# Kernel optimization log

Measured on AMD Instinct MI355X. Metric: run time of the kernel, lower is better.

## Reference

```python
import jax, jax.numpy as jnp
import numpy as np
import math

D, H, NQP, NKP = 512, 8, 4, 4
DH = D // H
OUT_DIM = D + H * NKP * 3  # 608


def setup_inputs() -> dict:
    key = jax.random.key(0)
    ks = jax.random.split(key, 12)
    B, L = 2, 1024
    s = jax.random.normal(ks[0], (B, L, D), dtype=jnp.float32)
    R = jax.random.normal(ks[1], (B, L, 3, 3), dtype=jnp.float32)
    tr = jax.random.normal(ks[2], (B, L, 3), dtype=jnp.float32)
    sc = 0.02
    Wq = jax.random.normal(ks[3], (D, D), dtype=jnp.float32) * sc
    Wk = jax.random.normal(ks[4], (D, D), dtype=jnp.float32) * sc
    Wv = jax.random.normal(ks[5], (D, D), dtype=jnp.float32) * sc
    Wqp = jax.random.normal(ks[6], (D, H * NQP * 3), dtype=jnp.float32) * sc
    Wkp = jax.random.normal(ks[7], (D, H * NKP * 3), dtype=jnp.float32) * sc
    Wvp = jax.random.normal(ks[8], (D, H * NKP * 3), dtype=jnp.float32) * sc
    Wo = jax.random.normal(ks[9], (OUT_DIM, D), dtype=jnp.float32) * sc
    bo = jnp.zeros((D,), dtype=jnp.float32)
    gamma = jnp.ones((D,), dtype=jnp.float32)
    beta = jnp.zeros((D,), dtype=jnp.float32)
    w_C = jnp.full((H,), math.log(20.0), dtype=jnp.float32)
    return dict(s=s, R=R, tr=tr, Wq=Wq, Wk=Wk, Wv=Wv, Wqp=Wqp, Wkp=Wkp,
                Wvp=Wvp, Wo=Wo, bo=bo, gamma=gamma, beta=beta, w_C=w_C)


def _layernorm(x, gamma, beta, eps=1e-5):
    mu = jnp.mean(x, axis=-1, keepdims=True)
    var = jnp.var(x, axis=-1, keepdims=True)
    return (x - mu) * jax.lax.rsqrt(var + eps) * gamma + beta


def reference(s, R, tr, Wq, Wk, Wv, Wqp, Wkp, Wvp, Wo, bo, gamma, beta, w_C):
    B, L, _ = s.shape
    # scalar q/k/v: (B, L, H, dh)
    Q = (s @ Wq).reshape(B, L, H, DH)
    K = (s @ Wk).reshape(B, L, H, DH)
    V = (s @ Wv).reshape(B, L, H, DH)
    a_s = jnp.einsum('bihd,bjhd->bhij', Q, K) / math.sqrt(DH)
    # local points: (B, L, H, P, 3)
    Qp = (s @ Wqp).reshape(B, L, H, NQP, 3)
    Kp = (s @ Wkp).reshape(B, L, H, NKP, 3)
    Vp = (s @ Wvp).reshape(B, L, H, NKP, 3)
    tr_e = tr[:, :, None, None, :]
    to_global = lambda p: jnp.einsum('blxy,blhpy->blhpx', R, p) + tr_e
    Qp_g, Kp_g, Vp_g = to_global(Qp), to_global(Kp), to_global(Vp)
    # (B, H, L, P, 3)
    qh = jnp.transpose(Qp_g, (0, 2, 1, 3, 4))
    kh = jnp.transpose(Kp_g, (0, 2, 1, 3, 4))
    diff = qh[:, :, :, None] - kh[:, :, None]          # (B,H,L,L,P,3)
    sq_dist = jnp.sum(diff * diff, axis=(-2, -1))      # (B,H,L,L)
    wc = jax.nn.softplus(w_C)[None, :, None, None]
    attn = jax.nn.softmax(a_s - 0.5 * wc * sq_dist, axis=-1)
    out_s = jnp.einsum('bhij,bjhd->bihd', attn, V).reshape(B, L, D)
    Vp_agg = jnp.einsum('bhij,bjhpc->bihpc', attn, Vp_g)  # (B,L,H,P,3)
    # global -> local: R^T (p - tr)
    Vp_local = jnp.einsum('blyx,blhpy->blhpx', R, Vp_agg - tr_e)
    out_p = Vp_local.reshape(B, L, H * NKP * 3)
    out = jnp.concatenate([out_s, out_p], axis=-1) @ Wo + bo
    return _layernorm(s + out, gamma, beta)
```

## Files before the change

### kernel.cpp

```cpp
#include <hip/hip_runtime.h>
#include <hip/hip_fp16.h>
#include <math.h>

typedef _Float16 f16;
typedef _Float16 f16x8 __attribute__((ext_vector_type(8)));
typedef _Float16 f16x4v __attribute__((ext_vector_type(4)));
typedef float f32x4 __attribute__((ext_vector_type(4)));

#define BATCH   2
#define LSEQ    1024
#define BLTOT   2048
#define DMODEL  512
#define NHEAD   8
#define PDIM    1824
#define AW      96
#define VW      80
#define ODIM    608
#define NSPLIT  2
#define OCPSTR  1310720

__global__ __launch_bounds__(256)
void prep_kernel(const float* __restrict__ s,
                 const float* __restrict__ Wq, const float* __restrict__ Wk,
                 const float* __restrict__ Wv, const float* __restrict__ Wqp,
                 const float* __restrict__ Wkp, const float* __restrict__ Wvp,
                 const float* __restrict__ Wo,
                 f16* __restrict__ sH, f16* __restrict__ WallT, f16* __restrict__ WoT)
{
    const int blk = blockIdx.x;
    const int t = threadIdx.x;
    __shared__ float tile[32][33];

    if (blk < 1024) {
        const int i = blk * 256 + t;
        float4 v = ((const float4*)s)[i];
        f16x4v o = { (f16)v.x, (f16)v.y, (f16)v.z, (f16)v.w };
        ((f16x4v*)sH)[i] = o;
        return;
    }
    if (blk < 1936) {
        const int idx = blk - 1024;
        const int n0 = (idx % 57) * 32, k0 = (idx / 57) * 32;
        const float* src; int ld, nc0;
        if      (n0 < 512)  { src = Wq;  ld = 512; nc0 = n0; }
        else if (n0 < 1024) { src = Wk;  ld = 512; nc0 = n0 - 512; }
        else if (n0 < 1536) { src = Wv;  ld = 512; nc0 = n0 - 1024; }
        else if (n0 < 1632) { src = Wqp; ld = 96;  nc0 = n0 - 1536; }
        else if (n0 < 1728) { src = Wkp; ld = 96;  nc0 = n0 - 1632; }
        else                { src = Wvp; ld = 96;  nc0 = n0 - 1728; }
#pragma unroll
        for (int i = 0; i < 4; ++i) {
            const int idx2 = t + i * 256;
            const int kl = idx2 >> 5, nl = idx2 & 31;
            tile[kl][nl] = src[(long long)(k0 + kl) * ld + nc0 + nl];
        }
        __syncthreads();
#pragma unroll
        for (int i = 0; i < 4; ++i) {
            const int idx2 = t + i * 256;
            const int nl = idx2 >> 5, kl = idx2 & 31;
            WallT[(long long)(n0 + nl) * 512 + k0 + kl] = (f16)tile[kl][nl];
        }
        return;
    }
    {
        const int idx = blk - 1936;
        const int n0 = (idx % 16) * 32, k0 = (idx / 16) * 32;
#pragma unroll
        for (int i = 0; i < 4; ++i) {
            const int idx2 = t + i * 256;
            const int kl = idx2 >> 5, nl = idx2 & 31;
            tile[kl][nl] = Wo[(long long)(k0 + kl) * 512 + n0 + nl];
        }
        __syncthreads();
#pragma unroll
        for (int i = 0; i < 4; ++i) {
            const int idx2 = t + i * 256;
            const int nl = idx2 >> 5, kl = idx2 & 31;
            WoT[(long long)(n0 + nl) * 608 + k0 + kl] = (f16)tile[kl][nl];
        }
    }
}

template<int BN, bool OUT16>
__global__ __launch_bounds__(256)
void gemm2_kernel(const f16* __restrict__ A, const f16* __restrict__ Bt,
                  void* __restrict__ Cout, int K, int ldc)
{
    constexpr int BCH = (BN * 4 + 255) / 256;
    __shared__ f16 As[2][64][40];
    __shared__ f16 Bs[2][BN][40];
    const int t = threadIdx.x;
    const int w = t >> 6, lane = t & 63, l15 = lane & 15, lhi = lane >> 4;
    const int row0 = blockIdx.y * 64, col0 = blockIdx.x * BN;
    const int ar = t >> 2, ac = t & 3;

    f32x4 acc[BN / 16];
#pragma unroll
    for (int n = 0; n < BN / 16; ++n) acc[n] = (f32x4){0.f, 0.f, 0.f, 0.f};

    const int nsteps = K >> 5;

    f16x8 aR;
    f16x8 bR[BCH];
    aR = *(const f16x8*)&A[(long long)(row0 + ar) * K + ac * 8];
#pragma unroll
    for (int i = 0; i < BCH; ++i) {
        const int cid = t + i * 256;
        if (cid < BN * 4) {
            const int br = cid >> 2, bc = cid & 3;
            bR[i] = *(const f16x8*)&Bt[(long long)(col0 + br) * K + bc * 8];
        }
    }
    *(f16x8*)&As[0][ar][ac * 8] = aR;
#pragma unroll
    for (int i = 0; i < BCH; ++i) {
        const int cid = t + i * 256;
        if (cid < BN * 4) *(f16x8*)&Bs[0][cid >> 2][(cid & 3) * 8] = bR[i];
    }
    __syncthreads();

    for (int st = 0; st < nsteps; ++st) {
        const int cur = st & 1;
        if (st + 1 < nsteps) {
            const int k0 = (st + 1) << 5;
            aR = *(const f16x8*)&A[(long long)(row0 + ar) * K + k0 + ac * 8];
#pragma unroll
            for (int i = 0; i < BCH; ++i) {
                const int cid = t + i * 256;
                if (cid < BN * 4) {
                    const int br = cid >> 2, bc = cid & 3;
                    bR[i] = *(const f16x8*)&Bt[(long long)(col0 + br) * K + k0 + bc * 8];
                }
            }
        }
        f16x8 af = *(const f16x8*)&As[cur][w * 16 + l15][lhi * 8];
        f16x8 bf[BN / 16];
#pragma unroll
        for (int n = 0; n < BN / 16; ++n)
            bf[n] = *(const f16x8*)&Bs[cur][n * 16 + l15][lhi * 8];
#pragma unroll
        for (int n = 0; n < BN / 16; ++n)
            acc[n] = __builtin_amdgcn_mfma_f32_16x16x32_f16(af, bf[n], acc[n], 0, 0, 0);
        if (st + 1 < nsteps) {
            *(f16x8*)&As[cur ^ 1][ar][ac * 8] = aR;
#pragma unroll
            for (int i = 0; i < BCH; ++i) {
                const int cid = t + i * 256;
                if (cid < BN * 4) *(f16x8*)&Bs[cur ^ 1][cid >> 2][(cid & 3) * 8] = bR[i];
            }
        }
        __syncthreads();
    }

    const int row = row0 + w * 16 + lhi * 4;
#pragma unroll
    for (int n = 0; n < BN / 16; ++n) {
        const int col = col0 + n * 16 + l15;
#pragma unroll
        for (int r = 0; r < 4; ++r) {
            if (OUT16) ((f16*)Cout)[(long long)(row + r) * ldc + col] = (f16)acc[n][r];
            else       ((float*)Cout)[(long long)(row + r) * ldc + col] = acc[n][r];
        }
    }
}

__global__ __launch_bounds__(256)
void build_aug2_kernel(const f16* __restrict__ P, const float* __restrict__ Rm,
                       const float* __restrict__ tr, const float* __restrict__ wC,
                       f16* __restrict__ QA, f16* __restrict__ KA,
                       f16* __restrict__ VCT, float* __restrict__ KOFF)
{
    const int l0 = blockIdx.x * 64;
    const int bh = blockIdx.y;
    const int b = bh >> 3, h = bh & 7;
    const int t = threadIdx.x;

    __shared__ float Rl[64][9];
    __shared__ float trl[64][3];
    __shared__ f16 gq[64][12];
    __shared__ f16 gk[64][12];
    __shared__ float k2[64][4];
    __shared__ f16 Vt[VW][72];
    __shared__ float wcs;

    const long long blbase = (long long)b * LSEQ + l0;

    for (int i = t; i < 64 * 9; i += 256) Rl[i / 9][i % 9] = Rm[blbase * 9 + i];
    for (int i = t; i < 64 * 3; i += 256) trl[i / 3][i % 3] = tr[blbase * 3 + i];
    if (t == 0) { float x = wC[h]; wcs = log1pf(expf(x)); }
    __syncthreads();
    const float wc = wcs;

    for (int i = t; i < 768; i += 256) {
        const int l = i / 12, pp = i - l * 12;
        const int proj = pp >> 2, p = pp & 3;
        const f16* src = P + (blbase + l) * PDIM + 1536 + proj * 96 + h * 12 + p * 3;
        const float x = (float)src[0], y = (float)src[1], z = (float)src[2];
        const float gx = Rl[l][0]*x + Rl[l][1]*y + Rl[l][2]*z + trl[l][0];
        const float gy = Rl[l][3]*x + Rl[l][4]*y + Rl[l][5]*z + trl[l][1];
        const float gz = Rl[l][6]*x + Rl[l][7]*y + Rl[l][8]*z + trl[l][2];
        if (proj == 0) {
            gq[l][p * 3 + 0] = (f16)(wc * gx);
            gq[l][p * 3 + 1] = (f16)(wc * gy);
            gq[l][p * 3 + 2] = (f16)(wc * gz);
        } else if (proj == 1) {
            gk[l][p * 3 + 0] = (f16)gx;
            gk[l][p * 3 + 1] = (f16)gy;
            gk[l][p * 3 + 2] = (f16)gz;
            k2[l][p] = gx * gx + gy * gy + gz * gz;
        } else {
            Vt[64 + p * 3 + 0][l] = (f16)gx;
            Vt[64 + p * 3 + 1][l] = (f16)gy;
            Vt[64 + p * 3 + 2][l] = (f16)gz;
        }
    }
    for (int i = t; i < 512; i += 256) {
        const int l = i >> 3, ch = i & 7;
        f16x8 v = *(const f16x8*)&P[(blbase + l) * PDIM + 1024 + h * 64 + ch * 8];
#pragma unroll
        for (int j = 0; j < 8; ++j) Vt[ch * 8 + j][l] = v[j];
    }
    for (int i = t; i < 36; i += 256) {
        const int r = 76 + i / 9, ch = i % 9;
        *(f16x8*)&Vt[r][ch * 8] = (f16x8){0,0,0,0,0,0,0,0};
    }
    __syncthreads();

    if (t < 64)
        KOFF[(long long)bh * LSEQ + l0 + t] =
            0.5f * wc * (k2[t][0] + k2[t][1] + k2[t][2] + k2[t][3]);

    for (int i = t; i < 768; i += 256) {
        const int l = i / 12, ch = i - l * 12;
        const long long prow = (blbase + l) * PDIM;
        const long long orow = ((long long)bh * LSEQ + l0 + l) * AW;
        f16x8 q, k;
        if (ch < 8) {
            f16x8 qv = *(const f16x8*)&P[prow + h * 64 + ch * 8];
            f16x8 kv = *(const f16x8*)&P[prow + 512 + h * 64 + ch * 8];
            q = qv * (f16)0.125f;
            k = kv;
        } else if (ch == 8) {
#pragma unroll
            for (int j = 0; j < 8; ++j) { q[j] = gq[l][j]; k[j] = gk[l][j]; }
        } else if (ch == 9) {
#pragma unroll
            for (int j = 0; j < 8; ++j) {
                q[j] = (j < 4) ? gq[l][8 + j] : (f16)0.f;
                k[j] = (j < 4) ? gk[l][8 + j] : (f16)0.f;
            }
        } else {
            q = (f16x8){0,0,0,0,0,0,0,0};
            k = (f16x8){0,0,0,0,0,0,0,0};
        }
        *(f16x8*)&QA[orow + ch * 8] = q;
        *(f16x8*)&KA[orow + ch * 8] = k;
    }
    for (int i = t; i < 640; i += 256) {
        const int c = i >> 3, lg = i & 7;
        *(f16x8*)&VCT[((long long)bh * VW + c) * LSEQ + l0 + lg * 8] =
            *(const f16x8*)&Vt[c][lg * 8];
    }
}

__global__ __launch_bounds__(256, 2)
void attn_kernel(const f16* __restrict__ QA, const f16* __restrict__ KA,
                 const f16* __restrict__ VCT, const float* __restrict__ KOFF,
                 f16* __restrict__ OCp, float2* __restrict__ ML)
{
    const int bh = blockIdx.y;
    const int q0 = blockIdx.x * 64;
    const int z  = blockIdx.z;
    const int t = threadIdx.x;
    const int w = t >> 6, lane = t & 63, l15 = lane & 15, lhi = lane >> 4;

    __shared__ f16 Ks[128][104];
    __shared__ f16 Vs[VW][136];
    __shared__ f16 Ps[64][136];

    const f16* qbase = QA + ((long long)bh * LSEQ + q0 + w * 16 + l15) * AW;
    f16x8 qf[3];
#pragma unroll
    for (int ks = 0; ks < 3; ++ks)
        qf[ks] = *(const f16x8*)(qbase + ks * 32 + lhi * 8);

    f32x4 Oacc[5];
#pragma unroll
    for (int nv = 0; nv < 5; ++nv) Oacc[nv] = (f32x4){0.f, 0.f, 0.f, 0.f};
    float M[4], L[4];
#pragma unroll
    for (int r = 0; r < 4; ++r) { M[r] = -1e30f; L[r] = 0.f; }

    const f16* kgbase = KA + (long long)bh * LSEQ * AW;
    const f16* vgbase = VCT + (long long)bh * VW * LSEQ;
    const float* koffb = KOFF + (long long)bh * LSEQ;

    const int kvbeg = z * (LSEQ / NSPLIT);
    const int kvend = kvbeg + LSEQ / NSPLIT;

#pragma unroll
    for (int i = 0; i < 6; ++i) {
        const int cid = t + i * 256;
        const int r = cid / 12, c = cid - r * 12;
        *(f16x8*)&Ks[r][c * 8] = *(const f16x8*)(kgbase + (long long)(kvbeg + r) * AW + c * 8);
    }
#pragma unroll
    for (int i = 0; i < 5; ++i) {
        const int cid = t + i * 256;
        const int r = cid >> 4, c = cid & 15;
        *(f16x8*)&Vs[r][c * 8] = *(const f16x8*)(vgbase + (long long)r * LSEQ + kvbeg + c * 8);
    }
    __syncthreads();

    for (int kv0 = kvbeg; kv0 < kvend; kv0 += 128) {
        const bool more = (kv0 + 128 < kvend);
        f16x8 kpre[6], vpre[5];
        if (more) {
#pragma unroll
            for (int i = 0; i < 6; ++i) {
                const int cid = t + i * 256;
                const int r = cid / 12, c = cid - r * 12;
                kpre[i] = *(const f16x8*)(kgbase + (long long)(kv0 + 128 + r) * AW + c * 8);
            }
#pragma unroll
            for (int i = 0; i < 5; ++i) {
                const int cid = t + i * 256;
                const int r = cid >> 4, c = cid & 15;
                vpre[i] = *(const f16x8*)(vgbase + (long long)r * LSEQ + kv0 + 128 + c * 8);
            }
        }

        f32x4 sc[8];
#pragma unroll
        for (int n = 0; n < 8; ++n) sc[n] = (f32x4){0.f, 0.f, 0.f, 0.f};
        __builtin_amdgcn_s_setprio(1);
#pragma unroll
        for (int n = 0; n < 8; ++n)
#pragma unroll
            for (int ks = 0; ks < 3; ++ks) {
                f16x8 kb = *(const f16x8*)&Ks[n * 16 + l15][ks * 32 + lhi * 8];
                sc[n] = __builtin_amdgcn_mfma_f32_16x16x32_f16(qf[ks], kb, sc[n], 0, 0, 0);
            }
        __builtin_amdgcn_s_setprio(0);
#pragma unroll
        for (int n = 0; n < 8; ++n) {
            const float ko = koffb[kv0 + n * 16 + l15];
#pragma unroll
            for (int r = 0; r < 4; ++r) sc[n][r] -= ko;
        }
        float sscale[4];
#pragma unroll
        for (int r = 0; r < 4; ++r) {
            float mr = sc[0][r];
#pragma unroll
            for (int n = 1; n < 8; ++n) mr = fmaxf(mr, sc[n][r]);
#pragma unroll
            for (int off = 1; off < 16; off <<= 1) mr = fmaxf(mr, __shfl_xor(mr, off));
            const float nm = fmaxf(M[r], mr);
            sscale[r] = __expf(M[r] - nm);
            M[r] = nm;
        }
        float rsum[4] = {0.f, 0.f, 0.f, 0.f};
#pragma unroll
        for (int n = 0; n < 8; ++n)
#pragma unroll
            for (int r = 0; r < 4; ++r) {
                const float p = __expf(sc[n][r] - M[r]);
                sc[n][r] = p;
                rsum[r] += p;
            }
#pragma unroll
        for (int r = 0; r < 4; ++r) {
            float s = rsum[r];
#pragma unroll
            for (int off = 1; off < 16; off <<= 1) s += __shfl_xor(s, off);
            L[r] = L[r] * sscale[r] + s;
        }
#pragma unroll
        for (int nv = 0; nv < 5; ++nv)
#pragma unroll
            for (int r = 0; r < 4; ++r) Oacc[nv][r] *= sscale[r];

#pragma unroll
        for (int n = 0; n < 8; ++n)
#pragma unroll
            for (int r = 0; r < 4; ++r)
                Ps[w * 16 + lhi * 4 + r][n * 16 + l15] = (f16)sc[n][r];

        f16x8 pa[4];
#pragma unroll
        for (int ks = 0; ks < 4; ++ks)
            pa[ks] = *(const f16x8*)&Ps[w * 16 + l15][ks * 32 + lhi * 8];
        __builtin_amdgcn_s_setprio(1);
#pragma unroll
        for (int nv = 0; nv < 5; ++nv)
#pragma unroll
            for (int ks = 0; ks < 4; ++ks) {
                f16x8 vb = *(const f16x8*)&Vs[nv * 16 + l15][ks * 32 + lhi * 8];
                Oacc[nv] = __builtin_amdgcn_mfma_f32_16x16x32_f16(pa[ks], vb, Oacc[nv], 0, 0, 0);
            }
        __builtin_amdgcn_s_setprio(0);
        __syncthreads();

        if (more) {
#pragma unroll
            for (int i = 0; i < 6; ++i) {
                const int cid = t + i * 256;
                const int r = cid / 12, c = cid - r * 12;
                *(f16x8*)&Ks[r][c * 8] = kpre[i];
            }
#pragma unroll
            for (int i = 0; i < 5; ++i) {
                const int cid = t + i * 256;
                const int r = cid >> 4, c = cid & 15;
                *(f16x8*)&Vs[r][c * 8] = vpre[i];
            }
        }
        __syncthreads();
    }

    f16* obase = OCp + (((long long)(z * 16 + bh) * LSEQ) + q0 + w * 16 + lhi * 4) * VW;
#pragma unroll
    for (int nv = 0; nv < 5; ++nv)
#pragma unroll
        for (int r = 0; r < 4; ++r)
            obase[r * VW + nv * 16 + l15] = (f16)Oacc[nv][r];
    if (l15 == 0) {
#pragma unroll
        for (int r = 0; r < 4; ++r)
            ML[(long long)(z * 16 + bh) * LSEQ + q0 + w * 16 + lhi * 4 + r] =
                make_float2(M[r], L[r]);
    }
}

__global__ __launch_bounds__(256)
void combine_concat_kernel(const f16* __restrict__ OCp, const float2* __restrict__ ML,
                           const float* __restrict__ Rm, const float* __restrict__ tr,
                           f16* __restrict__ CC)
{
    const int bl0 = blockIdx.x * 4;
    const int b = bl0 >> 10;
    const int t = threadIdx.x;

    __shared__ float w1s[4][8], w2s[4][8];
    if (t < 32) {
        const int row = t >> 3, h = t & 7;
        const int l = (bl0 + row) & 1023;
        const int bh = b * 8 + h;
        const float2 m1 = ML[(long long)bh * LSEQ + l];
        const float2 m2 = ML[(long long)(16 + bh) * LSEQ + l];
        const float mm = fmaxf(m1.x, m2.x);
        const float e1 = __expf(m1.x - mm), e2 = __expf(m2.x - mm);
        const float inv = 1.0f / (m1.y * e1 + m2.y * e2);
        w1s[row][h] = e1 * inv; w2s[row][h] = e2 * inv;
    }
    __syncthreads();

    for (int idx = t; idx < 2048; idx += 256) {
        const int row = idx >> 9, c = idx & 511;
        const int h = c >> 6, ch = c & 63;
        const int l = (bl0 + row) & 1023;
        const long long base = ((long long)(b * 8 + h) * LSEQ + l) * VW + ch;
        const float v = w1s[row][h] * (float)OCp[base] + w2s[row][h] * (float)OCp[OCPSTR + base];
        CC[(long long)(bl0 + row) * ODIM + c] = (f16)v;
    }
    if (t < 128) {
        const int row = t >> 5, h = (t >> 2) & 7, p = t & 3;
        const int bl = bl0 + row, l = bl & 1023;
        const long long base = ((long long)(b * 8 + h) * LSEQ + l) * VW + 64 + p * 3;
        const float w1 = w1s[row][h], w2 = w2s[row][h];
        float o[3];
#pragma unroll
        for (int c = 0; c < 3; ++c)
            o[c] = w1 * (float)OCp[base + c] + w2 * (float)OCp[OCPSTR + base + c]
                 - tr[(long long)bl * 3 + c];
        const float* Rr = Rm + (long long)bl * 9;
        f16* crow = CC + (long long)bl * ODIM + 512 + h * 12 + p * 3;
        crow[0] = (f16)(Rr[0]*o[0] + Rr[3]*o[1] + Rr[6]*o[2]);
        crow[1] = (f16)(Rr[1]*o[0] + Rr[4]*o[1] + Rr[7]*o[2]);
        crow[2] = (f16)(Rr[2]*o[0] + Rr[5]*o[1] + Rr[8]*o[2]);
    }
}

__global__ __launch_bounds__(256)
void residual_ln_kernel(const float* __restrict__ s, const float* __restrict__ Y,
                        const float* __restrict__ bo, const float* __restrict__ gamma,
                        const float* __restrict__ beta, float* __restrict__ out)
{
    const int bl = blockIdx.x;
    const int t = threadIdx.x;
    const float* srow = s + (long long)bl * DMODEL;
    const float* yrow = Y + (long long)bl * DMODEL;

    const float v0 = srow[t]       + yrow[t]       + bo[t];
    const float v1 = srow[t + 256] + yrow[t + 256] + bo[t + 256];

    float sum = v0 + v1, sq = v0 * v0 + v1 * v1;
#pragma unroll
    for (int o = 32; o > 0; o >>= 1) {
        sum += __shfl_xor(sum, o);
        sq  += __shfl_xor(sq,  o);
    }
    __shared__ float rs[4], rq[4];
    const int wid = t >> 6, lane = t & 63;
    if (lane == 0) { rs[wid] = sum; rq[wid] = sq; }
    __syncthreads();
    sum = rs[0] + rs[1] + rs[2] + rs[3];
    sq  = rq[0] + rq[1] + rq[2] + rq[3];

    const float mu  = sum * (1.0f / DMODEL);
    const float var = sq * (1.0f / DMODEL) - mu * mu;
    const float inv = rsqrtf(var + 1e-5f);

    out[(long long)bl * DMODEL + t]       = (v0 - mu) * inv * gamma[t]       + beta[t];
    out[(long long)bl * DMODEL + t + 256] = (v1 - mu) * inv * gamma[t + 256] + beta[t + 256];
}

extern "C" void kernel_launch(void* const* d_in, const int* in_sizes, int n_in,
                              void* d_out, int out_size, void* d_ws, size_t ws_size,
                              hipStream_t stream)
{
    const float* s    = (const float*)d_in[0];
    const float* R    = (const float*)d_in[1];
    const float* tr   = (const float*)d_in[2];
    const float* Wq   = (const float*)d_in[3];
    const float* Wk   = (const float*)d_in[4];
    const float* Wv   = (const float*)d_in[5];
    const float* Wqp  = (const float*)d_in[6];
    const float* Wkp  = (const float*)d_in[7];
    const float* Wvp  = (const float*)d_in[8];
    const float* Wo   = (const float*)d_in[9];
    const float* bo   = (const float*)d_in[10];
    const float* gam  = (const float*)d_in[11];
    const float* bet  = (const float*)d_in[12];
    const float* wC   = (const float*)d_in[13];
    float* out = (float*)d_out;

    f16* sH    = (f16*)d_ws;
    f16* WallT = sH + 1048576;
    f16* WoT   = WallT + 933888;
    f16* P     = WoT + 311296;
    f16* QA    = P + 3735552;
    f16* KA    = QA + 1572864;
    f16* VCT   = KA + 1572864;
    float* KOFF = (float*)(VCT + 1310720);
    f16* OCp    = (f16*)(KOFF + 16384);
    float2* ML  = (float2*)(OCp + 2621440);
    f16* CC     = (f16*)(ML + 32768);
    float* Y    = (float*)(CC + 1245184);

    const dim3 blk(256);

    prep_kernel<<<dim3(2240), blk, 0, stream>>>(s, Wq, Wk, Wv, Wqp, Wkp, Wvp, Wo,
                                                sH, WallT, WoT);

    gemm2_kernel<96, true><<<dim3(19, 32), blk, 0, stream>>>(sH, WallT, P, 512, 1824);

    build_aug2_kernel<<<dim3(16, 16), blk, 0, stream>>>(P, R, tr, wC, QA, KA, VCT, KOFF);

    attn_kernel<<<dim3(16, 16, NSPLIT), blk, 0, stream>>>(QA, KA, VCT, KOFF, OCp, ML);

    combine_concat_kernel<<<dim3(512), blk, 0, stream>>>(OCp, ML, R, tr, CC);

    gemm2_kernel<64, false><<<dim3(8, 32), blk, 0, stream>>>(CC, WoT, Y, 608, 512);

    residual_ln_kernel<<<dim3(BLTOT), blk, 0, stream>>>(s, Y, bo, gam, bet, out);
}
```

Baseline: 72.69 us.

## Fuse fp32-to-fp16 conversion into projection GEMM, add lazy softmax rescale, LSE combine

Removes the separate s-to-fp16 pass by loading fp32 s directly inside a new 128x96-tile projection GEMM. The attention kernel skips the running-max rescale when the new block max stays within 8 of the current max, normalizes its output in-kernel and writes log-sum-exp instead of (max, sum) pairs, which simplifies the split combine. The output GEMM is replaced with a 2x2-warp-tiled kernel. These changes cut kernel work and memory traffic, at the cost of more registers in the projection GEMM and a warp-divergent branch in the softmax loop.

```diff
diff --git a/kernel.cpp b/kernel.cpp
--- a/kernel.cpp
+++ b/kernel.cpp
@@ -20,27 +20,18 @@
 #define OCPSTR  1310720
 
 __global__ __launch_bounds__(256)
-void prep_kernel(const float* __restrict__ s,
-                 const float* __restrict__ Wq, const float* __restrict__ Wk,
+void prep_kernel(const float* __restrict__ Wq, const float* __restrict__ Wk,
                  const float* __restrict__ Wv, const float* __restrict__ Wqp,
                  const float* __restrict__ Wkp, const float* __restrict__ Wvp,
                  const float* __restrict__ Wo,
-                 f16* __restrict__ sH, f16* __restrict__ WallT, f16* __restrict__ WoT)
+                 f16* __restrict__ WallT, f16* __restrict__ WoT)
 {
     const int blk = blockIdx.x;
     const int t = threadIdx.x;
     __shared__ float tile[32][33];
 
-    if (blk < 1024) {
-        const int i = blk * 256 + t;
-        float4 v = ((const float4*)s)[i];
-        f16x4v o = { (f16)v.x, (f16)v.y, (f16)v.z, (f16)v.w };
-        ((f16x4v*)sH)[i] = o;
-        return;
-    }
-    if (blk < 1936) {
-        const int idx = blk - 1024;
-        const int n0 = (idx % 57) * 32, k0 = (idx / 57) * 32;
+    if (blk < 912) {
+        const int n0 = (blk % 57) * 32, k0 = (blk / 57) * 32;
         const float* src; int ld, nc0;
         if      (n0 < 512)  { src = Wq;  ld = 512; nc0 = n0; }
         else if (n0 < 1024) { src = Wk;  ld = 512; nc0 = n0 - 512; }
@@ -64,7 +55,7 @@
         return;
     }
     {
-        const int idx = blk - 1936;
+        const int idx = blk - 912;
         const int n0 = (idx % 16) * 32, k0 = (idx / 16) * 32;
 #pragma unroll
         for (int i = 0; i < 4; ++i) {
@@ -82,85 +73,114 @@
     }
 }
 
-template<int BN, bool OUT16>
 __global__ __launch_bounds__(256)
-void gemm2_kernel(const f16* __restrict__ A, const f16* __restrict__ Bt,
-                  void* __restrict__ Cout, int K, int ldc)
-{
-    constexpr int BCH = (BN * 4 + 255) / 256;
-    __shared__ f16 As[2][64][40];
-    __shared__ f16 Bs[2][BN][40];
+void proj_kernel(const float* __restrict__ s, const f16* __restrict__ WallT,
+                 f16* __restrict__ P)
+{
+    __shared__ f16 As[2][128][40];
+    __shared__ f16 Bs[2][96][40];
     const int t = threadIdx.x;
     const int w = t >> 6, lane = t & 63, l15 = lane & 15, lhi = lane >> 4;
-    const int row0 = blockIdx.y * 64, col0 = blockIdx.x * BN;
-    const int ar = t >> 2, ac = t & 3;
-
-    f32x4 acc[BN / 16];
-#pragma unroll
-    for (int n = 0; n < BN / 16; ++n) acc[n] = (f32x4){0.f, 0.f, 0.f, 0.f};
-
-    const int nsteps = K >> 5;
-
-    f16x8 aR;
-    f16x8 bR[BCH];
-    aR = *(const f16x8*)&A[(long long)(row0 + ar) * K + ac * 8];
-#pragma unroll
-    for (int i = 0; i < BCH; ++i) {
+    const int row0 = blockIdx.y * 128, col0 = blockIdx.x * 96;
+
+    f32x4 acc[2][6];
+#pragma unroll
+    for (int m = 0; m < 2; ++m)
+#pragma unroll
+        for (int n = 0; n < 6; ++n) acc[m][n] = (f32x4){0.f, 0.f, 0.f, 0.f};
+
+    float4 aR[2][2];
+    f16x8 bR[2];
+
+#pragma unroll
+    for (int i = 0; i < 2; ++i) {
         const int cid = t + i * 256;
-        if (cid < BN * 4) {
+        const int r = cid >> 2, c = cid & 3;
+        aR[i][0] = *(const float4*)&s[(long long)(row0 + r) * 512 + c * 8];
+        aR[i][1] = *(const float4*)&s[(long long)(row0 + r) * 512 + c * 8 + 4];
+    }
+#pragma unroll
+    for (int i = 0; i < 2; ++i) {
+        const int cid = t + i * 256;
+        if (cid < 384) {
             const int br = cid >> 2, bc = cid & 3;
-            bR[i] = *(const f16x8*)&Bt[(long long)(col0 + br) * K + bc * 8];
-        }
-    }
-    *(f16x8*)&As[0][ar][ac * 8] = aR;
-#pragma unroll
-    for (int i = 0; i < BCH; ++i) {
+            bR[i] = *(const f16x8*)&WallT[(long long)(col0 + br) * 512 + bc * 8];
+        }
+    }
+#pragma unroll
+    for (int i = 0; i < 2; ++i) {
         const int cid = t + i * 256;
-        if (cid < BN * 4) *(f16x8*)&Bs[0][cid >> 2][(cid & 3) * 8] = bR[i];
+        const int r = cid >> 2, c = cid & 3;
+        f16x8 v = { (f16)aR[i][0].x, (f16)aR[i][0].y, (f16)aR[i][0].z, (f16)aR[i][0].w,
+                    (f16)aR[i][1].x, (f16)aR[i][1].y, (f16)aR[i][1].z, (f16)aR[i][1].w };
+        *(f16x8*)&As[0][r][c * 8] = v;
+    }
+#pragma unroll
+    for (int i = 0; i < 2; ++i) {
+        const int cid = t + i * 256;
+        if (cid < 384) *(f16x8*)&Bs[0][cid >> 2][(cid & 3) * 8] = bR[i];
     }
     __syncthreads();
 
-    for (int st = 0; st < nsteps; ++st) {
+    for (int st = 0; st < 16; ++st) {
         const int cur = st & 1;
-        if (st + 1 < nsteps) {
+        if (st + 1 < 16) {
             const int k0 = (st + 1) << 5;
-            aR = *(const f16x8*)&A[(long long)(row0 + ar) * K + k0 + ac * 8];
-#pragma unroll
-            for (int i = 0; i < BCH; ++i) {
-                const int cid = t + i * 256;
-                if (cid < BN * 4) {
+#pragma unroll
+            for (int i = 0; i < 2; ++i) {
+                const int cid = t + i * 256;
+                const int r = cid >> 2, c = cid & 3;
+                aR[i][0] = *(const float4*)&s[(long long)(row0 + r) * 512 + k0 + c * 8];
+                aR[i][1] = *(const float4*)&s[(long long)(row0 + r) * 512 + k0 + c * 8 + 4];
+            }
+#pragma unroll
+            for (int i = 0; i < 2; ++i) {
+                const int cid = t + i * 256;
+                if (cid < 384) {
                     const int br = cid >> 2, bc = cid & 3;
-                    bR[i] = *(const f16x8*)&Bt[(long long)(col0 + br) * K + k0 + bc * 8];
+                    bR[i] = *(const f16x8*)&WallT[(long long)(col0 + br) * 512 + k0 + bc * 8];
                 }
             }
         }
-        f16x8 af = *(const f16x8*)&As[cur][w * 16 + l15][lhi * 8];
-        f16x8 bf[BN / 16];
-#pragma unroll
-        for (int n = 0; n < BN / 16; ++n)
+        f16x8 af[2], bf[6];
+#pragma unroll
+        for (int m = 0; m < 2; ++m)
+            af[m] = *(const f16x8*)&As[cur][w * 32 + m * 16 + l15][lhi * 8];
+#pragma unroll
+        for (int n = 0; n < 6; ++n)
             bf[n] = *(const f16x8*)&Bs[cur][n * 16 + l15][lhi * 8];
 #pragma unroll
-        for (int n = 0; n < BN / 16; ++n)
-            acc[n] = __builtin_amdgcn_mfma_f32_16x16x32_f16(af, bf[n], acc[n], 0, 0, 0);
-        if (st + 1 < nsteps) {
-            *(f16x8*)&As[cur ^ 1][ar][ac * 8] = aR;
-#pragma unroll
-            for (int i = 0; i < BCH; ++i) {
-                const int cid = t + i * 256;
-                if (cid < BN * 4) *(f16x8*)&Bs[cur ^ 1][cid >> 2][(cid & 3) * 8] = bR[i];
+        for (int m = 0; m < 2; ++m)
+#pragma unroll
+            for (int n = 0; n < 6; ++n)
+                acc[m][n] = __builtin_amdgcn_mfma_f32_16x16x32_f16(af[m], bf[n], acc[m][n], 0, 0, 0);
+        if (st + 1 < 16) {
+#pragma unroll
+            for (int i = 0; i < 2; ++i) {
+                const int cid = t + i * 256;
+                const int r = cid >> 2, c = cid & 3;
+                f16x8 v = { (f16)aR[i][0].x, (f16)aR[i][0].y, (f16)aR[i][0].z, (f16)aR[i][0].w,
+                            (f16)aR[i][1].x, (f16)aR[i][1].y, (f16)aR[i][1].z, (f16)aR[i][1].w };
+                *(f16x8*)&As[cur ^ 1][r][c * 8] = v;
+            }
+#pragma unroll
+            for (int i = 0; i < 2; ++i) {
+                const int cid = t + i * 256;
+                if (cid < 384) *(f16x8*)&Bs[cur ^ 1][cid >> 2][(cid & 3) * 8] = bR[i];
             }
         }
         __syncthreads();
     }
 
-    const int row = row0 + w * 16 + lhi * 4;
-#pragma unroll
-    for (int n = 0; n < BN / 16; ++n) {
-        const int col = col0 + n * 16 + l15;
-#pragma unroll
-        for (int r = 0; r < 4; ++r) {
-            if (OUT16) ((f16*)Cout)[(long long)(row + r) * ldc + col] = (f16)acc[n][r];
-            else       ((float*)Cout)[(long long)(row + r) * ldc + col] = acc[n][r];
+#pragma unroll
+    for (int m = 0; m < 2; ++m) {
+        const int row = row0 + w * 32 + m * 16 + lhi * 4;
+#pragma unroll
+        for (int n = 0; n < 6; ++n) {
+            const int col = col0 + n * 16 + l15;
+#pragma unroll
+            for (int r = 0; r < 4; ++r)
+                P[(long long)(row + r) * PDIM + col] = (f16)acc[m][n][r];
         }
     }
 }
@@ -267,7 +287,7 @@
 __global__ __launch_bounds__(256, 2)
 void attn_kernel(const f16* __restrict__ QA, const f16* __restrict__ KA,
                  const f16* __restrict__ VCT, const float* __restrict__ KOFF,
-                 f16* __restrict__ OCp, float2* __restrict__ ML)
+                 f16* __restrict__ OCp, float* __restrict__ LSE)
 {
     const int bh = blockIdx.y;
     const int q0 = blockIdx.x * 64;
@@ -349,38 +369,63 @@
 #pragma unroll
             for (int r = 0; r < 4; ++r) sc[n][r] -= ko;
         }
-        float sscale[4];
+        float mr[4];
 #pragma unroll
         for (int r = 0; r < 4; ++r) {
-            float mr = sc[0][r];
-#pragma unroll
-            for (int n = 1; n < 8; ++n) mr = fmaxf(mr, sc[n][r]);
-#pragma unroll
-            for (int off = 1; off < 16; off <<= 1) mr = fmaxf(mr, __shfl_xor(mr, off));
-            const float nm = fmaxf(M[r], mr);
-            sscale[r] = __expf(M[r] - nm);
-            M[r] = nm;
-        }
+            float m = sc[0][r];
+#pragma unroll
+            for (int n = 1; n < 8; ++n) m = fmaxf(m, sc[n][r]);
+#pragma unroll
+            for (int off = 1; off < 16; off <<= 1) m = fmaxf(m, __shfl_xor(m, off));
+            mr[r] = m;
+        }
+        const bool nog = (mr[0] <= M[0] + 8.f) && (mr[1] <= M[1] + 8.f) &&
+                         (mr[2] <= M[2] + 8.f) && (mr[3] <= M[3] + 8.f);
         float rsum[4] = {0.f, 0.f, 0.f, 0.f};
-#pragma unroll
-        for (int n = 0; n < 8; ++n)
+        if (__all(nog)) {
+#pragma unroll
+            for (int n = 0; n < 8; ++n)
+#pragma unroll
+                for (int r = 0; r < 4; ++r) {
+                    const float p = __expf(sc[n][r] - M[r]);
+                    sc[n][r] = p;
+                    rsum[r] += p;
+                }
 #pragma unroll
             for (int r = 0; r < 4; ++r) {
-                const float p = __expf(sc[n][r] - M[r]);
-                sc[n][r] = p;
-                rsum[r] += p;
-            }
-#pragma unroll
-        for (int r = 0; r < 4; ++r) {
-            float s = rsum[r];
-#pragma unroll
-            for (int off = 1; off < 16; off <<= 1) s += __shfl_xor(s, off);
-            L[r] = L[r] * sscale[r] + s;
-        }
-#pragma unroll
-        for (int nv = 0; nv < 5; ++nv)
-#pragma unroll
-            for (int r = 0; r < 4; ++r) Oacc[nv][r] *= sscale[r];
+                float s2 = rsum[r];
+#pragma unroll
+                for (int off = 1; off < 16; off <<= 1) s2 += __shfl_xor(s2, off);
+                L[r] += s2;
+            }
+        } else {
+            float sscale[4];
+#pragma unroll
+            for (int r = 0; r < 4; ++r) {
+                const float nm = fmaxf(M[r], mr[r]);
+                sscale[r] = __expf(M[r] - nm);
+                M[r] = nm;
+            }
+#pragma unroll
+            for (int n = 0; n < 8; ++n)
+#pragma unroll
+                for (int r = 0; r < 4; ++r) {
+                    const float p = __expf(sc[n][r] - M[r]);
+                    sc[n][r] = p;
+                    rsum[r] += p;
+                }
+#pragma unroll
+            for (int r = 0; r < 4; ++r) {
+                float s2 = rsum[r];
+#pragma unroll
+                for (int off = 1; off < 16; off <<= 1) s2 += __shfl_xor(s2, off);
+                L[r] = L[r] * sscale[r] + s2;
+            }
+#pragma unroll
+            for (int nv = 0; nv < 5; ++nv)
+#pragma unroll
+                for (int r = 0; r < 4; ++r) Oacc[nv][r] *= sscale[r];
+        }
 
 #pragma unroll
         for (int n = 0; n < 8; ++n)
@@ -420,22 +465,25 @@
         __syncthreads();
     }
 
+    float inv[4];
+#pragma unroll
+    for (int r = 0; r < 4; ++r) inv[r] = 1.0f / L[r];
     f16* obase = OCp + (((long long)(z * 16 + bh) * LSEQ) + q0 + w * 16 + lhi * 4) * VW;
 #pragma unroll
     for (int nv = 0; nv < 5; ++nv)
 #pragma unroll
         for (int r = 0; r < 4; ++r)
-            obase[r * VW + nv * 16 + l15] = (f16)Oacc[nv][r];
+            obase[r * VW + nv * 16 + l15] = (f16)(Oacc[nv][r] * inv[r]);
     if (l15 == 0) {
 #pragma unroll
         for (int r = 0; r < 4; ++r)
-            ML[(long long)(z * 16 + bh) * LSEQ + q0 + w * 16 + lhi * 4 + r] =
-                make_float2(M[r], L[r]);
+            LSE[(long long)(z * 16 + bh) * LSEQ + q0 + w * 16 + lhi * 4 + r] =
+                M[r] + __logf(L[r]);
     }
 }
 
 __global__ __launch_bounds__(256)
-void combine_concat_kernel(const f16* __restrict__ OCp, const float2* __restrict__ ML,
+void combine_concat_kernel(const f16* __restrict__ OCp, const float* __restrict__ LSE,
                            const float* __restrict__ Rm, const float* __restrict__ tr,
                            f16* __restrict__ CC)
 {
@@ -448,11 +496,11 @@
         const int row = t >> 3, h = t & 7;
         const int l = (bl0 + row) & 1023;
         const int bh = b * 8 + h;
-        const float2 m1 = ML[(long long)bh * LSEQ + l];
-        const float2 m2 = ML[(long long)(16 + bh) * LSEQ + l];
-        const float mm = fmaxf(m1.x, m2.x);
-        const float e1 = __expf(m1.x - mm), e2 = __expf(m2.x - mm);
-        const float inv = 1.0f / (m1.y * e1 + m2.y * e2);
+        const float l1 = LSE[(long long)bh * LSEQ + l];
+        const float l2 = LSE[(long long)(16 + bh) * LSEQ + l];
+        const float mm = fmaxf(l1, l2);
+        const float e1 = __expf(l1 - mm), e2 = __expf(l2 - mm);
+        const float inv = 1.0f / (e1 + e2);
         w1s[row][h] = e1 * inv; w2s[row][h] = e2 * inv;
     }
     __syncthreads();
@@ -480,6 +528,70 @@
         crow[0] = (f16)(Rr[0]*o[0] + Rr[3]*o[1] + Rr[6]*o[2]);
         crow[1] = (f16)(Rr[1]*o[0] + Rr[4]*o[1] + Rr[7]*o[2]);
         crow[2] = (f16)(Rr[2]*o[0] + Rr[5]*o[1] + Rr[8]*o[2]);
+    }
+}
+
+__global__ __launch_bounds__(256)
+void out_gemm_kernel(const f16* __restrict__ CC, const f16* __restrict__ WoT,
+                     float* __restrict__ Y)
+{
+    __shared__ f16 As[2][64][40];
+    __shared__ f16 Bs[2][64][40];
+    const int t = threadIdx.x;
+    const int w = t >> 6, lane = t & 63, l15 = lane & 15, lhi = lane >> 4;
+    const int wr = w >> 1, wc = w & 1;
+    const int row0 = blockIdx.y * 64, col0 = blockIdx.x * 64;
+    const int ar = t >> 2, ac = t & 3;
+
+    f32x4 acc[2][2];
+#pragma unroll
+    for (int m = 0; m < 2; ++m)
+#pragma unroll
+        for (int n = 0; n < 2; ++n) acc[m][n] = (f32x4){0.f, 0.f, 0.f, 0.f};
+
+    f16x8 aR, bR;
+    aR = *(const f16x8*)&CC[(long long)(row0 + ar) * ODIM + ac * 8];
+    bR = *(const f16x8*)&WoT[(long long)(col0 + ar) * ODIM + ac * 8];
+    *(f16x8*)&As[0][ar][ac * 8] = aR;
+    *(f16x8*)&Bs[0][ar][ac * 8] = bR;
+    __syncthreads();
+
+    for (int st = 0; st < 19; ++st) {
+        const int cur = st & 1;
+        if (st + 1 < 19) {
+            const int k0 = (st + 1) << 5;
+            aR = *(const f16x8*)&CC[(long long)(row0 + ar) * ODIM + k0 + ac * 8];
+            bR = *(const f16x8*)&WoT[(long long)(col0 + ar) * ODIM + k0 + ac * 8];
+        }
+        f16x8 af[2], bf[2];
+#pragma unroll
+        for (int m = 0; m < 2; ++m)
+            af[m] = *(const f16x8*)&As[cur][wr * 32 + m * 16 + l15][lhi * 8];
+#pragma unroll
+        for (int n = 0; n < 2; ++n)
+            bf[n] = *(const f16x8*)&Bs[cur][wc * 32 + n * 16 + l15][lhi * 8];
+#pragma unroll
+        for (int m = 0; m < 2; ++m)
+#pragma unroll
+            for (int n = 0; n < 2; ++n)
+                acc[m][n] = __builtin_amdgcn_mfma_f32_16x16x32_f16(af[m], bf[n], acc[m][n], 0, 0, 0);
+        if (st + 1 < 19) {
+            *(f16x8*)&As[cur ^ 1][ar][ac * 8] = aR;
+            *(f16x8*)&Bs[cur ^ 1][ar][ac * 8] = bR;
+        }
+        __syncthreads();
+    }
+
+#pragma unroll
+    for (int m = 0; m < 2; ++m) {
+        const int row = row0 + wr * 32 + m * 16 + lhi * 4;
+#pragma unroll
+        for (int n = 0; n < 2; ++n) {
+            const int col = col0 + wc * 32 + n * 16 + l15;
+#pragma unroll
+            for (int r = 0; r < 4; ++r)
+                Y[(long long)(row + r) * 512 + col] = acc[m][n][r];
+        }
     }
 }
 
@@ -537,8 +649,7 @@
     const float* wC   = (const float*)d_in[13];
     float* out = (float*)d_out;
 
-    f16* sH    = (f16*)d_ws;
-    f16* WallT = sH + 1048576;
+    f16* WallT = (f16*)d_ws;
     f16* WoT   = WallT + 933888;
     f16* P     = WoT + 311296;
     f16* QA    = P + 3735552;
@@ -546,24 +657,24 @@
     f16* VCT   = KA + 1572864;
     float* KOFF = (float*)(VCT + 1310720);
     f16* OCp    = (f16*)(KOFF + 16384);
-    float2* ML  = (float2*)(OCp + 2621440);
-    f16* CC     = (f16*)(ML + 32768);
+    float* LSE  = (float*)(OCp + 2621440);
+    f16* CC     = (f16*)(LSE + 32768);
     float* Y    = (float*)(CC + 1245184);
 
     const dim3 blk(256);
 
-    prep_kernel<<<dim3(2240), blk, 0, stream>>>(s, Wq, Wk, Wv, Wqp, Wkp, Wvp, Wo,
-                                                sH, WallT, WoT);
-
-    gemm2_kernel<96, true><<<dim3(19, 32), blk, 0, stream>>>(sH, WallT, P, 512, 1824);
+    prep_kernel<<<dim3(1216), blk, 0, stream>>>(Wq, Wk, Wv, Wqp, Wkp, Wvp, Wo,
+                                                WallT, WoT);
+
+    proj_kernel<<<dim3(19, 16), blk, 0, stream>>>(s, WallT, P);
 
     build_aug2_kernel<<<dim3(16, 16), blk, 0, stream>>>(P, R, tr, wC, QA, KA, VCT, KOFF);
 
-    attn_kernel<<<dim3(16, 16, NSPLIT), blk, 0, stream>>>(QA, KA, VCT, KOFF, OCp, ML);
-
-    combine_concat_kernel<<<dim3(512), blk, 0, stream>>>(OCp, ML, R, tr, CC);
-
-    gemm2_kernel<64, false><<<dim3(8, 32), blk, 0, stream>>>(CC, WoT, Y, 608, 512);
+    attn_kernel<<<dim3(16, 16, NSPLIT), blk, 0, stream>>>(QA, KA, VCT, KOFF, OCp, LSE);
+
+    combine_concat_kernel<<<dim3(512), blk, 0, stream>>>(OCp, LSE, R, tr, CC);
+
+    out_gemm_kernel<<<dim3(8, 32), blk, 0, stream>>>(CC, WoT, Y);
 
     residual_ln_kernel<<<dim3(BLTOT), blk, 0, stream>>>(s, Y, bo, gam, bet, out);
 }
```

After: 74.19 us. 2.1% more time.
